# Optimization experiments

Hardware: AMD Instinct MI355X
Metric: run time of the kernel (lower is better)

## Reference

```python
import jax, jax.numpy as jnp
import numpy as np


def setup_inputs() -> dict:
    key = jax.random.key(0)
    k1, k2, k3 = jax.random.split(key, 3)
    N, M, D = 8192, 16384, 24
    return {
        "x": jax.random.normal(k1, (M, D), dtype=jnp.float32),
        "samples": jax.random.normal(k2, (N, D), dtype=jnp.float32),
        "weights": jax.random.uniform(k3, (N,), dtype=jnp.float32),
        "sigma": jnp.ones((), dtype=jnp.float32),
        "length": jnp.ones((), dtype=jnp.float32),
    }


def reference(x, samples, weights, sigma, length):
    # Squared-exponential kernel K[n, m] = sigma^2 * exp(-||s_n - x_m||^2 / (2 l^2))
    # pairwise squared distances via ||s||^2 + ||x||^2 - 2 s.x  -> [N, M]
    s_sq = jnp.sum(samples * samples, axis=-1)[:, None]          # [N, 1]
    x_sq = jnp.sum(x * x, axis=-1)[None, :]                      # [1, M]
    cross = jnp.einsum("nd,md->nm", samples, x)                  # [N, M]
    sqdist = jnp.maximum(s_sq + x_sq - 2.0 * cross, 0.0)
    K = (sigma * sigma) * jnp.exp(-0.5 * sqdist / (length * length))  # [N, M]
    # torch.mv(K.T, weights).unsqueeze(1) -> [M, 1]
    out = jnp.einsum("nm,n->m", K, weights)[:, None]
    return out
```

## Files before the change

### kernel.cpp

```cpp
#include <hip/hip_runtime.h>


#define LOG2E_F 1.4426950408889634f

typedef __attribute__((ext_vector_type(8))) short bf16x8;
typedef __attribute__((ext_vector_type(4))) float f32x4;
typedef float v2f_ __attribute__((ext_vector_type(2)));

constexpr int D       = 24;
constexpr int KP      = 32;
constexpr int TILES   = 4;
constexpr int NSPLIT  = 32;
constexpr int TPB     = 256;
constexpr int TPB_PRE = 64;

__device__ inline unsigned short f32_to_bf16_rne(float f) {
    unsigned u = __builtin_bit_cast(unsigned, f);
    u += 0x7fffu + ((u >> 16) & 1u);
    return (unsigned short)(u >> 16);
}
__device__ inline float bf16_to_f32(unsigned short h) {
    unsigned u = ((unsigned)h) << 16;
    return __builtin_bit_cast(float, u);
}

constexpr unsigned short BF16_ONE = 0x3F80;

__global__ void prep_all(const float* __restrict__ x, const float* __restrict__ s,
                         const float* __restrict__ weights,
                         const float* __restrict__ sigma_p, const float* __restrict__ length_p,
                         unsigned short* __restrict__ xhi, unsigned short* __restrict__ xlo,
                         unsigned short* __restrict__ shi, unsigned short* __restrict__ slo,
                         float* __restrict__ out, int M, int N) {
    int i = blockIdx.x * blockDim.x + threadIdx.x;
    float l  = length_p[0];
    float c2 = -0.5f * LOG2E_F / (l * l);
    if (i < M) {
        out[i] = 0.f;
        const float* xr = x + (size_t)i * D;
        unsigned short hi[KP], lo[KP];
        float ssq = 0.f;
#pragma unroll
        for (int d = 0; d < D; ++d) {
            float v = xr[d];
            ssq = fmaf(v, v, ssq);
            unsigned short h = f32_to_bf16_rne(v);
            hi[d] = h;
            lo[d] = f32_to_bf16_rne(v - bf16_to_f32(h));
        }
#pragma unroll
        for (int d = D; d < KP; ++d) { hi[d] = 0; lo[d] = 0; }
        hi[24] = BF16_ONE; hi[25] = BF16_ONE;
        float cxv = c2 * ssq;
        unsigned short chi = f32_to_bf16_rne(cxv);
        hi[26] = chi;
        hi[27] = f32_to_bf16_rne(cxv - bf16_to_f32(chi));
#pragma unroll
        for (int q = 0; q < KP / 8; ++q) {
            bf16x8 vh, vl;
#pragma unroll
            for (int j = 0; j < 8; ++j) { vh[j] = (short)hi[q*8+j]; vl[j] = (short)lo[q*8+j]; }
            *reinterpret_cast<bf16x8*>(xhi + (size_t)i * KP + q * 8) = vh;
            *reinterpret_cast<bf16x8*>(xlo + (size_t)i * KP + q * 8) = vl;
        }
    } else if (i < M + N) {
        int n = i - M;
        float sg   = sigma_p[0];
        float m2c2 = -2.f * c2;
        const float* sr = s + (size_t)n * D;
        unsigned short hi[KP], lo[KP];
        float ssq = 0.f;
#pragma unroll
        for (int d = 0; d < D; ++d) {
            float v = sr[d];
            ssq = fmaf(v, v, ssq);
            float vs = m2c2 * v;
            unsigned short h = f32_to_bf16_rne(vs);
            hi[d] = h;
            lo[d] = f32_to_bf16_rne(vs - bf16_to_f32(h));
        }
#pragma unroll
        for (int d = D; d < KP; ++d) { hi[d] = 0; lo[d] = 0; }
        float lwt = __log2f(sg * sg * weights[n]) + c2 * ssq;
        lwt = fmaxf(lwt, -20000.f);
        unsigned short lhi = f32_to_bf16_rne(lwt);
        hi[24] = lhi;
        hi[25] = f32_to_bf16_rne(lwt - bf16_to_f32(lhi));
        hi[26] = BF16_ONE; hi[27] = BF16_ONE;
#pragma unroll
        for (int q = 0; q < KP / 8; ++q) {
            bf16x8 vh, vl;
#pragma unroll
            for (int j = 0; j < 8; ++j) { vh[j] = (short)hi[q*8+j]; vl[j] = (short)lo[q*8+j]; }
            *reinterpret_cast<bf16x8*>(shi + (size_t)n * KP + q * 8) = vh;
            *reinterpret_cast<bf16x8*>(slo + (size_t)n * KP + q * 8) = vl;
        }
    }
}

__global__ __launch_bounds__(TPB, 8) void ke_mfma(
    const unsigned short* __restrict__ xhi, const unsigned short* __restrict__ xlo,
    const unsigned short* __restrict__ shi, const unsigned short* __restrict__ slo,
    float* __restrict__ out, int M, int N) {
    int lane = threadIdx.x & 63;
    int wave = blockIdx.x * (TPB / 64) + (threadIdx.x >> 6);
    int MG   = M / (TILES * 16);
    int ns   = wave / MG;
    int mg   = wave - ns * MG;
    int m0   = mg * (TILES * 16);
    int r    = lane & 15;
    int q    = lane >> 4;

    bf16x8 bh[TILES], bl[TILES];
#pragma unroll
    for (int j = 0; j < TILES; ++j) {
        size_t xo = ((size_t)(m0 + j * 16 + r)) * KP + q * 8;
        bh[j] = *reinterpret_cast<const bf16x8*>(xhi + xo);
        bl[j] = *reinterpret_cast<const bf16x8*>(xlo + xo);
    }
#pragma unroll
    for (int j = 0; j < TILES; ++j) {
        asm("" : "+v"(bh[j]));
        asm("" : "+v"(bl[j]));
    }

    int per = (N / 16) / NSPLIT;
    int t0  = ns * per;

    const unsigned short* shp = shi + ((size_t)(t0 * 16 + r)) * KP + q * 8;
    const unsigned short* slp = slo + ((size_t)(t0 * 16 + r)) * KP + q * 8;

    float p[TILES] = {0.f, 0.f, 0.f, 0.f};
#pragma unroll 1
    for (int t = 0; t < per; ++t) {
        bf16x8 ah = *reinterpret_cast<const bf16x8*>(shp);
        bf16x8 al = *reinterpret_cast<const bf16x8*>(slp);
        shp += 16 * KP; slp += 16 * KP;
#pragma unroll
        for (int j = 0; j < TILES; ++j) {
            f32x4 z = {0.f, 0.f, 0.f, 0.f};
            f32x4 acc = __builtin_amdgcn_mfma_f32_16x16x32_bf16(ah, bh[j], z, 0, 0, 0);
            acc = __builtin_amdgcn_mfma_f32_16x16x32_bf16(al, bh[j], acc, 0, 0, 0);
            acc = __builtin_amdgcn_mfma_f32_16x16x32_bf16(ah, bl[j], acc, 0, 0, 0);
            float e0 = __builtin_amdgcn_exp2f(acc[0]);
            float e1 = __builtin_amdgcn_exp2f(acc[1]);
            float e2 = __builtin_amdgcn_exp2f(acc[2]);
            float e3 = __builtin_amdgcn_exp2f(acc[3]);
            p[j] += (e0 + e1) + (e2 + e3);
        }
    }
#pragma unroll
    for (int j = 0; j < TILES; ++j) {
        p[j] += __shfl_xor(p[j], 16, 64);
        p[j] += __shfl_xor(p[j], 32, 64);
    }
    if (lane < 16) {
#pragma unroll
        for (int j = 0; j < TILES; ++j)
            atomicAdd(&out[m0 + j * 16 + r], p[j]);
    }
}

constexpr int MPT  = 2;
constexpr int MBLK = TPB * MPT;

__global__ __launch_bounds__(TPB) void ke_plain(
    const float* __restrict__ x, const float* __restrict__ samples,
    const float* __restrict__ weights, const float* __restrict__ sigma_p,
    const float* __restrict__ length_p, float* __restrict__ out,
    int M, int N, int nsplit, int chunk) {
    int mb = blockIdx.x / nsplit;
    int ns = blockIdx.x - mb * nsplit;
    int t  = threadIdx.x;
    int m0 = mb * MBLK + t;
    int m1 = m0 + TPB;
    int m0c = (m0 < M) ? m0 : 0;
    int m1c = (m1 < M) ? m1 : 0;

    v2f_ xaq[D / 2], xbq[D / 2];
    const v2f_* xp0 = reinterpret_cast<const v2f_*>(x + (size_t)m0c * D);
    const v2f_* xp1 = reinterpret_cast<const v2f_*>(x + (size_t)m1c * D);
#pragma unroll
    for (int qq = 0; qq < D / 2; ++qq) { xaq[qq] = xp0[qq]; xbq[qq] = xp1[qq]; }
#pragma unroll
    for (int qq = 0; qq < D / 2; ++qq) { asm("" : "+v"(xaq[qq])); asm("" : "+v"(xbq[qq])); }

    float l   = length_p[0];
    float c   = -0.5f * LOG2E_F / (l * l);
    float m2c = -2.f * c;
    float sg  = sigma_p[0];
    float sg2 = sg * sg;

    v2f_ qa = {0.f, 0.f}, qb = {0.f, 0.f};
#pragma unroll
    for (int qq = 0; qq < D / 2; ++qq) {
        qa = __builtin_elementwise_fma(xaq[qq], xaq[qq], qa);
        qb = __builtin_elementwise_fma(xbq[qq], xbq[qq], qb);
    }
    float cxa = c * (qa.x + qa.y);
    float cxb = c * (qb.x + qb.y);

    float acc0 = 0.f, acc1 = 0.f;
    int n0 = ns * chunk;
    int n1 = n0 + chunk;
    if (n1 > N) n1 = N;
#pragma unroll 2
    for (int n = n0; n < n1; ++n) {
        const v2f_* s2 = reinterpret_cast<const v2f_*>(samples + (size_t)n * D);
        v2f_ da = {0.f, 0.f}, db = {0.f, 0.f}, sq = {0.f, 0.f};
#pragma unroll
        for (int qq = 0; qq < D / 2; ++qq) {
            v2f_ sv = s2[qq];
            sq = __builtin_elementwise_fma(sv, sv, sq);
            da = __builtin_elementwise_fma(sv, xaq[qq], da);
            db = __builtin_elementwise_fma(sv, xbq[qq], db);
        }
        float cn = c * (sq.x + sq.y);
        float wn = sg2 * weights[n];
        float e0 = fmaf(m2c, da.x + da.y, cn);
        float e1 = fmaf(m2c, db.x + db.y, cn);
        acc0 = fmaf(wn, __builtin_amdgcn_exp2f(e0), acc0);
        acc1 = fmaf(wn, __builtin_amdgcn_exp2f(e1), acc1);
    }
    if (m0 < M) atomicAdd(&out[m0], acc0 * __builtin_amdgcn_exp2f(cxa));
    if (m1 < M) atomicAdd(&out[m1], acc1 * __builtin_amdgcn_exp2f(cxb));
}

extern "C" void kernel_launch(void* const* d_in, const int* in_sizes, int n_in,
                              void* d_out, int out_size, void* d_ws, size_t ws_size,
                              hipStream_t stream) {
    const float* x       = (const float*)d_in[0];
    const float* samples = (const float*)d_in[1];
    const float* weights = (const float*)d_in[2];
    const float* sigma_p = (const float*)d_in[3];
    const float* length_p= (const float*)d_in[4];
    float* out = (float*)d_out;

    int M = in_sizes[0] / D;
    int N = in_sizes[1] / D;

    size_t xhi_off = 0;
    size_t xlo_off = xhi_off + (size_t)M * KP * 2;
    size_t shi_off = xlo_off + (size_t)M * KP * 2;
    size_t slo_off = shi_off + (size_t)N * KP * 2;
    size_t need    = slo_off + (size_t)N * KP * 2 + (size_t)16 * KP * 2;

    int  MT = TILES * 16;
    bool mfma_ok = ws_size >= need &&
                   (M % MT) == 0 && ((M / MT) % (TPB / 64)) == 0 &&
                   (N % 16) == 0 && ((N / 16) % NSPLIT) == 0 && out_size >= M;

    if (mfma_ok) {
        char* ws = (char*)d_ws;
        unsigned short* xhi = (unsigned short*)(ws + xhi_off);
        unsigned short* xlo = (unsigned short*)(ws + xlo_off);
        unsigned short* shi = (unsigned short*)(ws + shi_off);
        unsigned short* slo = (unsigned short*)(ws + slo_off);

        prep_all<<<dim3((M + N + TPB_PRE - 1) / TPB_PRE), dim3(TPB_PRE), 0, stream>>>(
            x, samples, weights, sigma_p, length_p, xhi, xlo, shi, slo, out, M, N);

        int waves  = (M / MT) * NSPLIT;
        int blocks = waves / (TPB / 64);
        ke_mfma<<<dim3(blocks), dim3(TPB), 0, stream>>>(
            xhi, xlo, shi, slo, out, M, N);
    } else {
        hipMemsetAsync(out, 0, (size_t)out_size * sizeof(float), stream);
        int mbcnt  = (M + MBLK - 1) / MBLK;
        int nsplit = 2048 / (mbcnt > 0 ? mbcnt : 1);
        if (nsplit < 1) nsplit = 1;
        if (nsplit > N) nsplit = N;
        int chunk = (N + nsplit - 1) / nsplit;
        ke_plain<<<dim3(mbcnt * nsplit), dim3(TPB), 0, stream>>>(
            x, samples, weights, sigma_p, length_p, out, M, N, nsplit, chunk);
    }
}
```

Baseline: 35.41 us.

## Fuse bf16 split preprocessing into MFMA kernel via shared-memory staging

Removes the separate prep kernel and global workspace. Each block now loads its 256 x rows and 256 sample rows from fp32, splits them into hi/lo bf16 in shared memory, and runs the MFMA/exp2 loop from LDS. A memset zeroes the output. This saves a kernel launch and the workspace round trip, but every block redoes sample preprocessing (recomputed per M group) and the path requires N to equal exactly 8192.

```diff
diff --git a/kernel.cpp b/kernel.cpp
--- a/kernel.cpp
+++ b/kernel.cpp
@@ -7,12 +7,11 @@
 typedef __attribute__((ext_vector_type(4))) float f32x4;
 typedef float v2f_ __attribute__((ext_vector_type(2)));
 
-constexpr int D       = 24;
-constexpr int KP      = 32;
-constexpr int TILES   = 4;
-constexpr int NSPLIT  = 32;
-constexpr int TPB     = 256;
-constexpr int TPB_PRE = 64;
+constexpr int D      = 24;
+constexpr int TILES  = 4;
+constexpr int NSPLIT = 32;
+constexpr int CT     = 16;
+constexpr int TPB    = 256;
 
 __device__ inline unsigned short f32_to_bf16_rne(float f) {
     unsigned u = __builtin_bit_cast(unsigned, f);
@@ -26,116 +25,95 @@
 
 constexpr unsigned short BF16_ONE = 0x3F80;
 
-__global__ void prep_all(const float* __restrict__ x, const float* __restrict__ s,
-                         const float* __restrict__ weights,
-                         const float* __restrict__ sigma_p, const float* __restrict__ length_p,
-                         unsigned short* __restrict__ xhi, unsigned short* __restrict__ xlo,
-                         unsigned short* __restrict__ shi, unsigned short* __restrict__ slo,
-                         float* __restrict__ out, int M, int N) {
-    int i = blockIdx.x * blockDim.x + threadIdx.x;
-    float l  = length_p[0];
-    float c2 = -0.5f * LOG2E_F / (l * l);
-    if (i < M) {
-        out[i] = 0.f;
-        const float* xr = x + (size_t)i * D;
-        unsigned short hi[KP], lo[KP];
-        float ssq = 0.f;
-#pragma unroll
-        for (int d = 0; d < D; ++d) {
-            float v = xr[d];
-            ssq = fmaf(v, v, ssq);
-            unsigned short h = f32_to_bf16_rne(v);
-            hi[d] = h;
-            lo[d] = f32_to_bf16_rne(v - bf16_to_f32(h));
-        }
-#pragma unroll
-        for (int d = D; d < KP; ++d) { hi[d] = 0; lo[d] = 0; }
-        hi[24] = BF16_ONE; hi[25] = BF16_ONE;
-        float cxv = c2 * ssq;
-        unsigned short chi = f32_to_bf16_rne(cxv);
-        hi[26] = chi;
-        hi[27] = f32_to_bf16_rne(cxv - bf16_to_f32(chi));
-#pragma unroll
-        for (int q = 0; q < KP / 8; ++q) {
-            bf16x8 vh, vl;
-#pragma unroll
-            for (int j = 0; j < 8; ++j) { vh[j] = (short)hi[q*8+j]; vl[j] = (short)lo[q*8+j]; }
-            *reinterpret_cast<bf16x8*>(xhi + (size_t)i * KP + q * 8) = vh;
-            *reinterpret_cast<bf16x8*>(xlo + (size_t)i * KP + q * 8) = vl;
-        }
-    } else if (i < M + N) {
-        int n = i - M;
-        float sg   = sigma_p[0];
-        float m2c2 = -2.f * c2;
-        const float* sr = s + (size_t)n * D;
-        unsigned short hi[KP], lo[KP];
-        float ssq = 0.f;
-#pragma unroll
-        for (int d = 0; d < D; ++d) {
-            float v = sr[d];
-            ssq = fmaf(v, v, ssq);
-            float vs = m2c2 * v;
-            unsigned short h = f32_to_bf16_rne(vs);
-            hi[d] = h;
-            lo[d] = f32_to_bf16_rne(vs - bf16_to_f32(h));
-        }
-#pragma unroll
-        for (int d = D; d < KP; ++d) { hi[d] = 0; lo[d] = 0; }
-        float lwt = __log2f(sg * sg * weights[n]) + c2 * ssq;
+__device__ inline float load_row24(const float* __restrict__ src, float* v) {
+    float ssq = 0.f;
+#pragma unroll
+    for (int i = 0; i < 6; ++i) {
+        float4 f = reinterpret_cast<const float4*>(src)[i];
+        v[4*i+0] = f.x; v[4*i+1] = f.y; v[4*i+2] = f.z; v[4*i+3] = f.w;
+    }
+#pragma unroll
+    for (int d = 0; d < 24; ++d) ssq = fmaf(v[d], v[d], ssq);
+    return ssq;
+}
+
+__device__ inline void stage_row(unsigned short* __restrict__ sm, int t,
+                                 const float* __restrict__ v, float scale,
+                                 float splitval, bool split_at_26) {
+    unsigned short hi[32], lo[32];
+#pragma unroll
+    for (int d = 0; d < 24; ++d) {
+        float vs = scale * v[d];
+        unsigned short h = f32_to_bf16_rne(vs);
+        hi[d] = h;
+        lo[d] = f32_to_bf16_rne(vs - bf16_to_f32(h));
+    }
+    unsigned short shv = f32_to_bf16_rne(splitval);
+    unsigned short slv = f32_to_bf16_rne(splitval - bf16_to_f32(shv));
+    if (split_at_26) { hi[24] = BF16_ONE; hi[25] = BF16_ONE; hi[26] = shv; hi[27] = slv; }
+    else             { hi[24] = shv; hi[25] = slv; hi[26] = BF16_ONE; hi[27] = BF16_ONE; }
+    hi[28] = 0; hi[29] = 0; hi[30] = 0; hi[31] = 0;
+#pragma unroll
+    for (int d = 24; d < 32; ++d) lo[d] = 0;
+    int sb = (t >> 4) * 512 + (t & 15) * 8;
+#pragma unroll
+    for (int q2 = 0; q2 < 4; ++q2) {
+        bf16x8 vh, vl;
+#pragma unroll
+        for (int j2 = 0; j2 < 8; ++j2) { vh[j2] = (short)hi[q2*8+j2]; vl[j2] = (short)lo[q2*8+j2]; }
+        *reinterpret_cast<bf16x8*>(sm + sb + q2 * 128) = vh;
+        *reinterpret_cast<bf16x8*>(sm + 8192 + sb + q2 * 128) = vl;
+    }
+}
+
+__global__ __launch_bounds__(TPB, 5) void ke_fused(
+    const float* __restrict__ x, const float* __restrict__ s,
+    const float* __restrict__ wts,
+    const float* __restrict__ sigma_p, const float* __restrict__ length_p,
+    float* __restrict__ out, int M, int N, int MGRP) {
+    __shared__ __align__(16) unsigned short sm[16384];
+    int t    = threadIdx.x;
+    int lane = t & 63;
+    int wv   = t >> 6;
+    int mg   = blockIdx.x % MGRP;
+    int ns   = blockIdx.x / MGRP;
+    int r    = lane & 15;
+
+    float l    = length_p[0];
+    float c2   = -0.5f * LOG2E_F / (l * l);
+    float m2c2 = -2.f * c2;
+    float sg   = sigma_p[0];
+
+    float v[24];
+    {
+        int row = mg * 256 + t;
+        float ssq = load_row24(x + (size_t)row * D, v);
+        stage_row(sm, t, v, 1.f, c2 * ssq, true);
+    }
+    __syncthreads();
+    bf16x8 bh[TILES], bl[TILES];
+#pragma unroll
+    for (int j = 0; j < TILES; ++j) {
+        int si = ((wv * 4 + j) * 64 + lane) * 8;
+        bh[j] = *reinterpret_cast<const bf16x8*>(sm + si);
+        bl[j] = *reinterpret_cast<const bf16x8*>(sm + 8192 + si);
+    }
+#pragma unroll
+    for (int j = 0; j < TILES; ++j) { asm("" : "+v"(bh[j]), "+v"(bl[j])); }
+    __syncthreads();
+    {
+        int row = ns * 256 + t;
+        float ssq = load_row24(s + (size_t)row * D, v);
+        float lwt = __log2f(sg * sg * wts[row]) + c2 * ssq;
         lwt = fmaxf(lwt, -20000.f);
-        unsigned short lhi = f32_to_bf16_rne(lwt);
-        hi[24] = lhi;
-        hi[25] = f32_to_bf16_rne(lwt - bf16_to_f32(lhi));
-        hi[26] = BF16_ONE; hi[27] = BF16_ONE;
-#pragma unroll
-        for (int q = 0; q < KP / 8; ++q) {
-            bf16x8 vh, vl;
-#pragma unroll
-            for (int j = 0; j < 8; ++j) { vh[j] = (short)hi[q*8+j]; vl[j] = (short)lo[q*8+j]; }
-            *reinterpret_cast<bf16x8*>(shi + (size_t)n * KP + q * 8) = vh;
-            *reinterpret_cast<bf16x8*>(slo + (size_t)n * KP + q * 8) = vl;
-        }
-    }
-}
-
-__global__ __launch_bounds__(TPB, 8) void ke_mfma(
-    const unsigned short* __restrict__ xhi, const unsigned short* __restrict__ xlo,
-    const unsigned short* __restrict__ shi, const unsigned short* __restrict__ slo,
-    float* __restrict__ out, int M, int N) {
-    int lane = threadIdx.x & 63;
-    int wave = blockIdx.x * (TPB / 64) + (threadIdx.x >> 6);
-    int MG   = M / (TILES * 16);
-    int ns   = wave / MG;
-    int mg   = wave - ns * MG;
-    int m0   = mg * (TILES * 16);
-    int r    = lane & 15;
-    int q    = lane >> 4;
-
-    bf16x8 bh[TILES], bl[TILES];
-#pragma unroll
-    for (int j = 0; j < TILES; ++j) {
-        size_t xo = ((size_t)(m0 + j * 16 + r)) * KP + q * 8;
-        bh[j] = *reinterpret_cast<const bf16x8*>(xhi + xo);
-        bl[j] = *reinterpret_cast<const bf16x8*>(xlo + xo);
-    }
-#pragma unroll
-    for (int j = 0; j < TILES; ++j) {
-        asm("" : "+v"(bh[j]));
-        asm("" : "+v"(bl[j]));
-    }
-
-    int per = (N / 16) / NSPLIT;
-    int t0  = ns * per;
-
-    const unsigned short* shp = shi + ((size_t)(t0 * 16 + r)) * KP + q * 8;
-    const unsigned short* slp = slo + ((size_t)(t0 * 16 + r)) * KP + q * 8;
-
+        stage_row(sm, t, v, m2c2, lwt, false);
+    }
+    __syncthreads();
     float p[TILES] = {0.f, 0.f, 0.f, 0.f};
 #pragma unroll 1
-    for (int t = 0; t < per; ++t) {
-        bf16x8 ah = *reinterpret_cast<const bf16x8*>(shp);
-        bf16x8 al = *reinterpret_cast<const bf16x8*>(slp);
-        shp += 16 * KP; slp += 16 * KP;
+    for (int tt = 0; tt < CT; ++tt) {
+        bf16x8 ah = *reinterpret_cast<const bf16x8*>(sm + (tt * 64 + lane) * 8);
+        bf16x8 al = *reinterpret_cast<const bf16x8*>(sm + 8192 + (tt * 64 + lane) * 8);
 #pragma unroll
         for (int j = 0; j < TILES; ++j) {
             f32x4 z = {0.f, 0.f, 0.f, 0.f};
@@ -155,6 +133,7 @@
         p[j] += __shfl_xor(p[j], 32, 64);
     }
     if (lane < 16) {
+        int m0 = mg * 256 + wv * 64;
 #pragma unroll
         for (int j = 0; j < TILES; ++j)
             atomicAdd(&out[m0 + j * 16 + r], p[j]);
@@ -239,33 +218,16 @@
     int M = in_sizes[0] / D;
     int N = in_sizes[1] / D;
 
-    size_t xhi_off = 0;
-    size_t xlo_off = xhi_off + (size_t)M * KP * 2;
-    size_t shi_off = xlo_off + (size_t)M * KP * 2;
-    size_t slo_off = shi_off + (size_t)N * KP * 2;
-    size_t need    = slo_off + (size_t)N * KP * 2 + (size_t)16 * KP * 2;
-
-    int  MT = TILES * 16;
-    bool mfma_ok = ws_size >= need &&
-                   (M % MT) == 0 && ((M / MT) % (TPB / 64)) == 0 &&
-                   (N % 16) == 0 && ((N / 16) % NSPLIT) == 0 && out_size >= M;
-
-    if (mfma_ok) {
-        char* ws = (char*)d_ws;
-        unsigned short* xhi = (unsigned short*)(ws + xhi_off);
-        unsigned short* xlo = (unsigned short*)(ws + xlo_off);
-        unsigned short* shi = (unsigned short*)(ws + shi_off);
-        unsigned short* slo = (unsigned short*)(ws + slo_off);
-
-        prep_all<<<dim3((M + N + TPB_PRE - 1) / TPB_PRE), dim3(TPB_PRE), 0, stream>>>(
-            x, samples, weights, sigma_p, length_p, xhi, xlo, shi, slo, out, M, N);
-
-        int waves  = (M / MT) * NSPLIT;
-        int blocks = waves / (TPB / 64);
-        ke_mfma<<<dim3(blocks), dim3(TPB), 0, stream>>>(
-            xhi, xlo, shi, slo, out, M, N);
+    hipMemsetAsync(out, 0, (size_t)out_size * sizeof(float), stream);
+
+    bool fused_ok = (M % 256) == 0 && (N == NSPLIT * CT * 16) && out_size >= M;
+
+    if (fused_ok) {
+        int MGRP   = M / 256;
+        int blocks = MGRP * NSPLIT;
+        ke_fused<<<dim3(blocks), dim3(TPB), 0, stream>>>(
+            x, samples, weights, sigma_p, length_p, out, M, N, MGRP);
     } else {
-        hipMemsetAsync(out, 0, (size_t)out_size * sizeof(float), stream);
         int mbcnt  = (M + MBLK - 1) / MBLK;
         int nsplit = 2048 / (mbcnt > 0 ? mbcnt : 1);
         if (nsplit < 1) nsplit = 1;
```

Result: slower. 36.78 us (+3.9%).
